# Optimization experiments

Hardware: AMD Instinct MI355X
Metric: run time of the kernel (lower is better)

The kernel has to match this reference:

```python
import jax, jax.numpy as jnp
import numpy as np


def setup_inputs() -> dict:
    key = jax.random.key(0)
    k1, k2, k3, k4 = jax.random.split(key, 4)
    B, S, D = 32, 2048, 128
    queries = jax.random.normal(k1, (B, S, D), dtype=jnp.float32)
    keys = jax.random.normal(k2, (B, S, D), dtype=jnp.float32)
    values = jax.random.normal(k3, (B, S, D), dtype=jnp.float32)
    mask = jax.random.randint(k4, (B, 1, S), 0, 2, dtype=jnp.int32)
    return {"queries": queries, "keys": keys, "values": values, "mask": mask}


def reference(queries, keys, values, mask):
    # scores: [B, Sq, Sk]
    scores = jnp.einsum("bqd,bkd->bqk", queries, keys)
    pad = (mask == 0)  # broadcasts [B,1,Sk] over queries
    min_value = jnp.finfo(scores.dtype).min
    scores = jnp.where(pad, min_value, scores)
    attn = jax.nn.softmax(scores, axis=-1)
    attn = jnp.where(pad, jnp.array(0.0, attn.dtype), attn)
    return jnp.einsum("bqk,bkd->bqd", attn, values)
```

## Files before the change

### kernel.cpp

```cpp
#include <hip/hip_runtime.h>
#include <stdint.h>

#define Bb 32
#define Ss 2048
#define Dd 128
#define KVB 64
#define NIT (Ss / KVB)

typedef __attribute__((ext_vector_type(2))) float f32x2;
typedef __attribute__((ext_vector_type(4))) float f32x4;
typedef __attribute__((ext_vector_type(16))) float f32x16;
typedef __attribute__((ext_vector_type(8))) _Float16 f16x8;
typedef __attribute__((ext_vector_type(2))) __fp16 fp16x2;
typedef __attribute__((ext_vector_type(8))) unsigned short u16x8;
typedef __attribute__((ext_vector_type(4))) unsigned short u16x4;

union F16_8 { u16x8 u; uint32_t w[4]; f16x8 h; };
union F16_4 { u16x4 u; uint32_t w[2]; };

__device__ __forceinline__ uint32_t pk2(float a, float b) {
    union { fp16x2 h; uint32_t u; } v;
    v.h = __builtin_amdgcn_cvt_pkrtz(a, b);
    return v.u;
}

__global__ __launch_bounds__(256)
void attn_prep(const float* __restrict__ K, const float* __restrict__ V,
               const int* __restrict__ M,
               unsigned short* __restrict__ Kc, unsigned short* __restrict__ Vc,
               int* __restrict__ CNT) {
    __shared__ int scan_s[256];
    __shared__ unsigned short idx_l[Ss];
    const int b = blockIdx.x >> 5, chunk = blockIdx.x & 31;
    const int tid = threadIdx.x;

    const int* m = M + (size_t)b * Ss + tid * 8;
    int loc[8]; int csum = 0;
    {
        int4 a = *(const int4*)m;
        int4 c = *(const int4*)(m + 4);
        loc[0] = (a.x != 0); loc[1] = (a.y != 0); loc[2] = (a.z != 0); loc[3] = (a.w != 0);
        loc[4] = (c.x != 0); loc[5] = (c.y != 0); loc[6] = (c.z != 0); loc[7] = (c.w != 0);
#pragma unroll
        for (int j = 0; j < 8; ++j) csum += loc[j];
    }
    scan_s[tid] = csum;
    __syncthreads();
    for (int off = 1; off < 256; off <<= 1) {
        int v = scan_s[tid];
        int u = (tid >= off) ? scan_s[tid - off] : 0;
        __syncthreads();
        scan_s[tid] = v + u;
        __syncthreads();
    }
    const int count = scan_s[255];
    {
        int base = scan_s[tid] - csum;
#pragma unroll
        for (int j = 0; j < 8; ++j)
            if (loc[j]) idx_l[base++] = (unsigned short)(tid * 8 + j);
    }
    __syncthreads();
    if (chunk == 0 && tid == 0) CNT[b] = count;

    const int ntpad = ((count + 63) >> 6) << 6;
    const int p0 = chunk * 64;
    if (p0 >= ntpad) return;

    const int rsub = tid >> 4;
    const int colh = (tid & 15) * 8;
    const size_t gbase = (size_t)b * Ss * Dd;
#pragma unroll
    for (int pass = 0; pass < 2; ++pass) {
        const float* src = pass ? V : K;
        unsigned short* dst = pass ? Vc : Kc;
#pragma unroll
        for (int it = 0; it < 4; ++it) {
            int s = p0 + rsub + it * 16;
            if (s >= ntpad) continue;
            F16_8 t;
            if (s < count) {
                const float* sp = src + gbase + (size_t)idx_l[s] * Dd + colh;
                f32x4 x = *(const f32x4*)sp;
                f32x4 y = *(const f32x4*)(sp + 4);
                t.w[0] = pk2(x[0], x[1]); t.w[1] = pk2(x[2], x[3]);
                t.w[2] = pk2(y[0], y[1]); t.w[3] = pk2(y[2], y[3]);
            } else {
                t.w[0] = 0u; t.w[1] = 0u; t.w[2] = 0u; t.w[3] = 0u;
            }
            *(u16x8*)(dst + gbase + (size_t)s * Dd + colh) = t.u;
        }
    }
}

__global__ __launch_bounds__(256) __attribute__((amdgpu_waves_per_eu(2, 2)))
void attn_fwd_d(const float* __restrict__ Q,
                const unsigned short* __restrict__ Kc,
                const unsigned short* __restrict__ Vc,
                const int* __restrict__ CNT,
                float* __restrict__ O) {
    __shared__ unsigned short K_lds[2][KVB * 128];
    __shared__ unsigned short VT_lds[2][128 * 64];
    __shared__ float maskadd[KVB];

    const int tid = threadIdx.x;
    const int w   = tid >> 6;
    const int l   = tid & 63;
    const int q31 = l & 31;
    const int hi  = l >> 5;

    const int bid   = blockIdx.x;
    const int batch = (bid & 7) * 4 + (bid >> 7);
    const int qtile = (bid >> 3) & 15;

    const size_t qrow0 = (size_t)batch * Ss + qtile * 128 + w * 32;
    const size_t kvb16 = (size_t)batch * Ss * Dd;

    const int count = CNT[batch];
    const int ntile = (count + KVB - 1) >> 6;

    const int grow = tid >> 4;
    const int gs   = tid & 15;
    auto gloadK = [&](int bf, int kv) {
#pragma unroll
        for (int it = 0; it < 4; ++it) {
            const int r = it * 16 + grow;
            const unsigned short* src = Kc + kvb16 + (size_t)(kv + r) * Dd + ((gs ^ (r & 7)) << 3);
            void* dst = (char*)(&K_lds[bf][0]) + it * 4096 + w * 1024;
            __builtin_amdgcn_global_load_lds(
                (const __attribute__((address_space(1))) uint32_t*)src,
                (__attribute__((address_space(3))) uint32_t*)dst, 16, 0, 0);
        }
    };

    const int vi = tid & 15;
    const int vk = (tid >> 4) << 2;
    uint32_t vv[4][4];

    auto issueV = [&](int kv) {
#pragma unroll
        for (int j = 0; j < 4; ++j)
#pragma unroll
            for (int ko = 0; ko < 4; ++ko)
                vv[j][ko] = *(const uint32_t*)(Vc + kvb16 + (size_t)(kv + vk + ko) * Dd + 2 * vi + 32 * j);
    };
    auto writeV = [&](int bf) {
#pragma unroll
        for (int j = 0; j < 4; ++j)
#pragma unroll
            for (int p = 0; p < 2; ++p) {
                int row = 2 * vi + p + 32 * j;
                F16_4 t;
                if (p == 0) {
                    t.w[0] = (vv[j][0] & 0xffffu) | (vv[j][1] << 16);
                    t.w[1] = (vv[j][2] & 0xffffu) | (vv[j][3] << 16);
                } else {
                    t.w[0] = (vv[j][0] >> 16) | (vv[j][1] & 0xffff0000u);
                    t.w[1] = (vv[j][2] >> 16) | (vv[j][3] & 0xffff0000u);
                }
                *(u16x4*)&VT_lds[bf][row * 64 + (vk ^ ((row & 7) << 3))] = t.u;
            }
    };

    F16_8 ones;
    {
        uint32_t ow = (q31 < 8) ? 0x3C003C00u : 0u;
        ones.w[0] = ow; ones.w[1] = ow; ones.w[2] = ow; ones.w[3] = ow;
    }

    const f32x16 z16 = {0,0,0,0,0,0,0,0,0,0,0,0,0,0,0,0};
    f32x16 acco[4];
#pragma unroll
    for (int dn = 0; dn < 4; ++dn) acco[dn] = z16;
    f32x16 accl = z16;
    float mrun = -1e4f;

    const float LOG2E = 1.44269504088896340736f;
    if (ntile > 0) { gloadK(0, 0); issueV(0); }
    if (tid < KVB) maskadd[tid] = ((ntile - 1) * KVB + tid < count) ? 0.f : -1e30f;
    F16_8 qf[8];
#pragma unroll
    for (int ks = 0; ks < 8; ++ks) {
        const float* s = Q + (qrow0 + q31) * Dd + ks * 16 + hi * 8;
        f32x4 a = *(const f32x4*)s;
        f32x4 b = *(const f32x4*)(s + 4);
        qf[ks].w[0] = pk2(a[0] * LOG2E, a[1] * LOG2E);
        qf[ks].w[1] = pk2(a[2] * LOG2E, a[3] * LOG2E);
        qf[ks].w[2] = pk2(b[0] * LOG2E, b[1] * LOG2E);
        qf[ks].w[3] = pk2(b[2] * LOG2E, b[3] * LOG2E);
    }
    if (ntile > 0) {
        writeV(0);
        __syncthreads();
    }

    for (int t = 0; t < ntile; ++t) {
        const int bf = t & 1;
        const bool pf = (t + 1 < ntile);
        if (pf) { gloadK(bf ^ 1, (t + 1) * KVB); issueV((t + 1) * KVB); }

        f32x16 accs[2];
        accs[0] = z16; accs[1] = z16;
#pragma unroll
        for (int ks = 0; ks < 8; ++ks) {
#pragma unroll
            for (int n = 0; n < 2; ++n) {
                int row = n * 32 + q31;
                F16_8 kf;
                kf.u = *(const u16x8*)&K_lds[bf][(row * 128 + ks * 16 + hi * 8) ^ ((row & 7) << 3)];
                accs[n] = __builtin_amdgcn_mfma_f32_32x32x16_f16(kf.h, qf[ks].h, accs[n], 0, 0, 0);
            }
        }

        if ((t == ntile - 1) && (count & 63)) {
#pragma unroll
            for (int n = 0; n < 2; ++n)
#pragma unroll
                for (int blk = 0; blk < 4; ++blk) {
                    f32x4 md = *(const f32x4*)&maskadd[n * 32 + blk * 8 + 4 * hi];
#pragma unroll
                    for (int r = 0; r < 4; ++r) accs[n][blk * 4 + r] += md[r];
                }
        }

        float mx[16];
#pragma unroll
        for (int i = 0; i < 16; ++i) mx[i] = fmaxf(accs[0][i], accs[1][i]);
#pragma unroll
        for (int s = 8; s >= 1; s >>= 1)
#pragma unroll
            for (int i = 0; i < s; ++i) mx[i] = fmaxf(mx[i], mx[i + s]);
        float pmax = fmaxf(mx[0], __shfl_xor(mx[0], 32));

        if (!__all(pmax - mrun <= 11.5409f)) {
            float mnew = fmaxf(mrun, pmax);
            float sc = __builtin_amdgcn_exp2f(mrun - mnew);
#pragma unroll
            for (int dn = 0; dn < 4; ++dn)
#pragma unroll
                for (int i = 0; i < 16; ++i) acco[dn][i] *= sc;
            accl[0] *= sc;
            mrun = mnew;
        }

#pragma unroll
        for (int n = 0; n < 2; ++n)
#pragma unroll
            for (int i = 0; i < 16; ++i) accs[n][i] = __builtin_amdgcn_exp2f(accs[n][i] - mrun);

        F16_8 pa[4];
#pragma unroll
        for (int ks = 0; ks < 4; ++ks) {
            int n  = ks >> 1;
            int b4 = (ks & 1) * 8;
            uint32_t x0 = pk2(accs[n][b4 + 0], accs[n][b4 + 1]);
            uint32_t x1 = pk2(accs[n][b4 + 2], accs[n][b4 + 3]);
            uint32_t y0 = pk2(accs[n][b4 + 4], accs[n][b4 + 5]);
            uint32_t y1 = pk2(accs[n][b4 + 6], accs[n][b4 + 7]);
            asm volatile("v_permlane32_swap_b32 %0, %1" : "+v"(x0), "+v"(y0));
            asm volatile("v_permlane32_swap_b32 %0, %1" : "+v"(x1), "+v"(y1));
            pa[ks].w[0] = x0; pa[ks].w[1] = x1; pa[ks].w[2] = y0; pa[ks].w[3] = y1;
        }

        if (pf) writeV(bf ^ 1);

#pragma unroll
        for (int dn = 0; dn < 4; ++dn) {
            int row = dn * 32 + q31;
#pragma unroll
            for (int ks = 0; ks < 4; ++ks) {
                F16_8 vf;
                vf.u = *(const u16x8*)&VT_lds[bf][row * 64 + ((ks * 16 + hi * 8) ^ ((row & 7) << 3))];
                acco[dn] = __builtin_amdgcn_mfma_f32_32x32x16_f16(vf.h, pa[ks].h, acco[dn], 0, 0, 0);
            }
        }
#pragma unroll
        for (int ks = 0; ks < 4; ++ks)
            accl = __builtin_amdgcn_mfma_f32_32x32x16_f16(ones.h, pa[ks].h, accl, 0, 0, 0);

        if (pf) __syncthreads();
    }

    float lv   = accl[0];
    float linv = lv > 0.f ? 1.0f / lv : 0.f;
    float* orow = O + (qrow0 + q31) * Dd;
#pragma unroll
    for (int dn = 0; dn < 4; ++dn)
#pragma unroll
        for (int rg = 0; rg < 4; ++rg) {
            f32x4 o;
            o[0] = acco[dn][rg * 4 + 0] * linv;
            o[1] = acco[dn][rg * 4 + 1] * linv;
            o[2] = acco[dn][rg * 4 + 2] * linv;
            o[3] = acco[dn][rg * 4 + 3] * linv;
            *(f32x4*)(orow + dn * 32 + rg * 8 + 4 * hi) = o;
        }
}

__global__ __launch_bounds__(256) __attribute__((amdgpu_waves_per_eu(2, 2)))
void attn_fwd(const float* __restrict__ Q,
              const float* __restrict__ K,
              const float* __restrict__ V,
              const int* __restrict__ M,
              float* __restrict__ O) {
    __shared__ unsigned short K_lds[KVB * 128];
    __shared__ unsigned short VT_lds[128 * 64];
    __shared__ float maskadd[KVB];

    const int tid = threadIdx.x;
    const int w   = tid >> 6;
    const int l   = tid & 63;
    const int q31 = l & 31;
    const int hi  = l >> 5;

    const int bid   = blockIdx.x;
    const int batch = (bid & 7) * 4 + (bid >> 7);
    const int qtile = (bid >> 3) & 15;

    const size_t qrow0  = (size_t)batch * Ss + qtile * 128 + w * 32;
    const size_t kvbase = (size_t)batch * Ss * Dd;
    const size_t mbase  = (size_t)batch * Ss;

    const int krow = tid >> 4;
    const int kcol = (tid & 15) << 3;
    const int vi   = tid & 15;
    const int vk   = (tid >> 4) << 2;

    f32x4 ka[4], kb[4];
    f32x2 vv[4][4];
    int mld = 0;

    auto issueK = [&](int kv) {
#pragma unroll
        for (int it = 0; it < 4; ++it) {
            const float* s = K + kvbase + (size_t)(kv + krow + it * 16) * Dd + kcol;
            ka[it] = *(const f32x4*)s;
            kb[it] = *(const f32x4*)(s + 4);
        }
        if (tid < KVB) mld = M[mbase + kv + tid];
    };
    auto writeK = [&]() {
#pragma unroll
        for (int it = 0; it < 4; ++it) {
            int row = krow + it * 16;
            F16_8 t;
            t.w[0] = pk2(ka[it][0], ka[it][1]);
            t.w[1] = pk2(ka[it][2], ka[it][3]);
            t.w[2] = pk2(kb[it][0], kb[it][1]);
            t.w[3] = pk2(kb[it][2], kb[it][3]);
            *(u16x8*)&K_lds[(row * 128 + kcol) ^ ((row & 7) << 3)] = t.u;
        }
        if (tid < KVB) maskadd[tid] = mld ? 0.f : -1e30f;
    };
    auto issueV = [&](int kv) {
#pragma unroll
        for (int j = 0; j < 4; ++j)
#pragma unroll
            for (int ko = 0; ko < 4; ++ko)
                vv[j][ko] = *(const f32x2*)(V + kvbase + (size_t)(kv + vk + ko) * Dd + 2 * vi + 32 * j);
    };
    auto writeV = [&]() {
#pragma unroll
        for (int j = 0; j < 4; ++j)
#pragma unroll
            for (int p = 0; p < 2; ++p) {
                int row = 2 * vi + p + 32 * j;
                F16_4 t;
                t.w[0] = pk2(vv[j][0][p], vv[j][1][p]);
                t.w[1] = pk2(vv[j][2][p], vv[j][3][p]);
                *(u16x4*)&VT_lds[row * 64 + (vk ^ ((row & 7) << 3))] = t.u;
            }
    };

    F16_8 ones;
    {
        uint32_t ow = (q31 < 8) ? 0x3C003C00u : 0u;
        ones.w[0] = ow; ones.w[1] = ow; ones.w[2] = ow; ones.w[3] = ow;
    }

    const f32x16 z16 = {0,0,0,0,0,0,0,0,0,0,0,0,0,0,0,0};
    f32x16 acco[4];
#pragma unroll
    for (int dn = 0; dn < 4; ++dn) acco[dn] = z16;
    f32x16 accl = z16;
    float mrun = -1e4f;

    const float LOG2E = 1.44269504088896340736f;
    issueK(0); issueV(0);
    F16_8 qf[8];
#pragma unroll
    for (int ks = 0; ks < 8; ++ks) {
        const float* s = Q + (qrow0 + q31) * Dd + ks * 16 + hi * 8;
        f32x4 a = *(const f32x4*)s;
        f32x4 b = *(const f32x4*)(s + 4);
        qf[ks].w[0] = pk2(a[0] * LOG2E, a[1] * LOG2E);
        qf[ks].w[1] = pk2(a[2] * LOG2E, a[3] * LOG2E);
        qf[ks].w[2] = pk2(b[0] * LOG2E, b[1] * LOG2E);
        qf[ks].w[3] = pk2(b[2] * LOG2E, b[3] * LOG2E);
    }
    writeK(); writeV();
    __syncthreads();

    for (int t = 0; t < NIT; ++t) {
        if (t < NIT - 1) issueK((t + 1) * KVB);

        f32x16 accs[2];
        accs[0] = z16; accs[1] = z16;
#pragma unroll
        for (int ks = 0; ks < 8; ++ks) {
#pragma unroll
            for (int n = 0; n < 2; ++n) {
                int row = n * 32 + q31;
                F16_8 kf;
                kf.u = *(const u16x8*)&K_lds[(row * 128 + ks * 16 + hi * 8) ^ ((row & 7) << 3)];
                accs[n] = __builtin_amdgcn_mfma_f32_32x32x16_f16(kf.h, qf[ks].h, accs[n], 0, 0, 0);
            }
        }

#pragma unroll
        for (int n = 0; n < 2; ++n)
#pragma unroll
            for (int blk = 0; blk < 4; ++blk) {
                f32x4 md = *(const f32x4*)&maskadd[n * 32 + blk * 8 + 4 * hi];
#pragma unroll
                for (int r = 0; r < 4; ++r) accs[n][blk * 4 + r] += md[r];
            }

        float mx[16];
#pragma unroll
        for (int i = 0; i < 16; ++i) mx[i] = fmaxf(accs[0][i], accs[1][i]);
#pragma unroll
        for (int s = 8; s >= 1; s >>= 1)
#pragma unroll
            for (int i = 0; i < s; ++i) mx[i] = fmaxf(mx[i], mx[i + s]);
        float pmax = fmaxf(mx[0], __shfl_xor(mx[0], 32));

        if (!__all(pmax - mrun <= 11.5409f)) {
            float mnew = fmaxf(mrun, pmax);
            float sc = __builtin_amdgcn_exp2f(mrun - mnew);
#pragma unroll
            for (int dn = 0; dn < 4; ++dn)
#pragma unroll
                for (int i = 0; i < 16; ++i) acco[dn][i] *= sc;
            accl[0] *= sc;
            mrun = mnew;
        }

#pragma unroll
        for (int n = 0; n < 2; ++n)
#pragma unroll
            for (int i = 0; i < 16; ++i) accs[n][i] = __builtin_amdgcn_exp2f(accs[n][i] - mrun);

        F16_8 pa[4];
#pragma unroll
        for (int ks = 0; ks < 4; ++ks) {
            int n  = ks >> 1;
            int b4 = (ks & 1) * 8;
            uint32_t x0 = pk2(accs[n][b4 + 0], accs[n][b4 + 1]);
            uint32_t x1 = pk2(accs[n][b4 + 2], accs[n][b4 + 3]);
            uint32_t y0 = pk2(accs[n][b4 + 4], accs[n][b4 + 5]);
            uint32_t y1 = pk2(accs[n][b4 + 6], accs[n][b4 + 7]);
            asm volatile("v_permlane32_swap_b32 %0, %1" : "+v"(x0), "+v"(y0));
            asm volatile("v_permlane32_swap_b32 %0, %1" : "+v"(x1), "+v"(y1));
            pa[ks].w[0] = x0; pa[ks].w[1] = x1; pa[ks].w[2] = y0; pa[ks].w[3] = y1;
        }

        __syncthreads();
        if (t < NIT - 1) { writeK(); issueV((t + 1) * KVB); }

#pragma unroll
        for (int dn = 0; dn < 4; ++dn) {
            int row = dn * 32 + q31;
#pragma unroll
            for (int ks = 0; ks < 4; ++ks) {
                F16_8 vf;
                vf.u = *(const u16x8*)&VT_lds[row * 64 + ((ks * 16 + hi * 8) ^ ((row & 7) << 3))];
                acco[dn] = __builtin_amdgcn_mfma_f32_32x32x16_f16(vf.h, pa[ks].h, acco[dn], 0, 0, 0);
            }
        }
#pragma unroll
        for (int ks = 0; ks < 4; ++ks)
            accl = __builtin_amdgcn_mfma_f32_32x32x16_f16(ones.h, pa[ks].h, accl, 0, 0, 0);

        __syncthreads();
        if (t < NIT - 1) writeV();
    }

    float lv   = accl[0];
    float linv = lv > 0.f ? 1.0f / lv : 0.f;
    float* orow = O + (qrow0 + q31) * Dd;
#pragma unroll
    for (int dn = 0; dn < 4; ++dn)
#pragma unroll
        for (int rg = 0; rg < 4; ++rg) {
            f32x4 o;
            o[0] = acco[dn][rg * 4 + 0] * linv;
            o[1] = acco[dn][rg * 4 + 1] * linv;
            o[2] = acco[dn][rg * 4 + 2] * linv;
            o[3] = acco[dn][rg * 4 + 3] * linv;
            *(f32x4*)(orow + dn * 32 + rg * 8 + 4 * hi) = o;
        }
}

extern "C" void kernel_launch(void* const* d_in, const int* in_sizes, int n_in,
                              void* d_out, int out_size, void* d_ws, size_t ws_size,
                              hipStream_t stream) {
    const float* Q = (const float*)d_in[0];
    const float* K = (const float*)d_in[1];
    const float* V = (const float*)d_in[2];
    const int*   M = (const int*)d_in[3];
    float* O = (float*)d_out;

    const size_t nKV  = (size_t)Bb * Ss * Dd;
    const size_t need = nKV * 2 * 2 + (size_t)Bb * 4;

    if (d_ws != nullptr && ws_size >= need) {
        unsigned short* Kc  = (unsigned short*)d_ws;
        unsigned short* Vc  = Kc + nKV;
        int*            CNT = (int*)(Vc + nKV);
        attn_prep<<<dim3(Bb * 32), dim3(256), 0, stream>>>(K, V, M, Kc, Vc, CNT);
        attn_fwd_d<<<dim3(Bb * (Ss / 128)), dim3(256), 0, stream>>>(Q, Kc, Vc, CNT, O);
    } else {
        attn_fwd<<<dim3(Bb * (Ss / 128)), dim3(256), 0, stream>>>(Q, K, V, M, O);
    }
}
```

Before: 69.61 us.

## Pre-pack K and V into MFMA fragment order in prep kernel

The prep kernel now writes compacted K and V tiles directly in the per-lane MFMA fragment layout, with V transposed through shared memory. The attention kernel then loads both tiles with direct global-to-LDS copies and reads fragments at linear offsets. This removes the register staging and in-kernel V transpose, the swizzle arithmetic, and the mask-add LDS array, which is replaced by a per-element compare. The cost is a heavier prep kernel with an LDS transpose that has strided 16-bit reads likely to hit bank conflicts, plus a remapped batch order in prep.

```diff
diff --git a/kernel.cpp b/kernel.cpp
--- a/kernel.cpp
+++ b/kernel.cpp
@@ -27,11 +27,15 @@
 __global__ __launch_bounds__(256)
 void attn_prep(const float* __restrict__ K, const float* __restrict__ V,
                const int* __restrict__ M,
-               unsigned short* __restrict__ Kc, unsigned short* __restrict__ Vc,
+               unsigned short* __restrict__ Kf, unsigned short* __restrict__ Vf,
                int* __restrict__ CNT) {
     __shared__ int scan_s[256];
     __shared__ unsigned short idx_l[Ss];
-    const int b = blockIdx.x >> 5, chunk = blockIdx.x & 31;
+    __shared__ unsigned short vt[KVB * 128];
+
+    const int x = blockIdx.x;
+    const int b     = ((x & 7) << 2) | ((x >> 3) & 3);
+    const int chunk = x >> 5;
     const int tid = threadIdx.x;
 
     const int* m = M + (size_t)b * Ss + tid * 8;
@@ -63,45 +67,79 @@
     __syncthreads();
     if (chunk == 0 && tid == 0) CNT[b] = count;
 
-    const int ntpad = ((count + 63) >> 6) << 6;
-    const int p0 = chunk * 64;
-    if (p0 >= ntpad) return;
-
-    const int rsub = tid >> 4;
-    const int colh = (tid & 15) * 8;
+    const int ntile = (count + 63) >> 6;
+    if (chunk >= ntile) return;
+
+    const int kb = chunk * 64;
     const size_t gbase = (size_t)b * Ss * Dd;
-#pragma unroll
-    for (int pass = 0; pass < 2; ++pass) {
-        const float* src = pass ? V : K;
-        unsigned short* dst = pass ? Vc : Kc;
+    const size_t fbase = ((size_t)b * 32 + chunk) * 8192;
+
+#pragma unroll
+    for (int j = 0; j < 4; ++j) {
+        const int o  = tid + 256 * j;
+        const int l  = o & 63;
+        const int fn = o >> 6;
+        const int ks = fn >> 1, n = fn & 1;
+        const int s  = kb + n * 32 + (l & 31);
+        const int d0 = ks * 16 + (l >> 5) * 8;
+        F16_8 t;
+        if (s < count) {
+            const float* sp = K + gbase + (size_t)idx_l[s] * Dd + d0;
+            f32x4 xv = *(const f32x4*)sp;
+            f32x4 yv = *(const f32x4*)(sp + 4);
+            t.w[0] = pk2(xv[0], xv[1]); t.w[1] = pk2(xv[2], xv[3]);
+            t.w[2] = pk2(yv[0], yv[1]); t.w[3] = pk2(yv[2], yv[3]);
+        } else {
+            t.w[0] = 0u; t.w[1] = 0u; t.w[2] = 0u; t.w[3] = 0u;
+        }
+        *(u16x8*)(Kf + fbase + (size_t)o * 8) = t.u;
+    }
+
+    {
+        const int rsub = tid >> 4;
+        const int colh = (tid & 15) * 8;
 #pragma unroll
         for (int it = 0; it < 4; ++it) {
-            int s = p0 + rsub + it * 16;
-            if (s >= ntpad) continue;
+            const int row = rsub + it * 16;
+            const int s   = kb + row;
             F16_8 t;
             if (s < count) {
-                const float* sp = src + gbase + (size_t)idx_l[s] * Dd + colh;
-                f32x4 x = *(const f32x4*)sp;
-                f32x4 y = *(const f32x4*)(sp + 4);
-                t.w[0] = pk2(x[0], x[1]); t.w[1] = pk2(x[2], x[3]);
-                t.w[2] = pk2(y[0], y[1]); t.w[3] = pk2(y[2], y[3]);
+                const float* sp = V + gbase + (size_t)idx_l[s] * Dd + colh;
+                f32x4 xv = *(const f32x4*)sp;
+                f32x4 yv = *(const f32x4*)(sp + 4);
+                t.w[0] = pk2(xv[0], xv[1]); t.w[1] = pk2(xv[2], xv[3]);
+                t.w[2] = pk2(yv[0], yv[1]); t.w[3] = pk2(yv[2], yv[3]);
             } else {
                 t.w[0] = 0u; t.w[1] = 0u; t.w[2] = 0u; t.w[3] = 0u;
             }
-            *(u16x8*)(dst + gbase + (size_t)s * Dd + colh) = t.u;
-        }
+            *(u16x8*)&vt[row * 128 + colh] = t.u;
+        }
+    }
+    __syncthreads();
+
+#pragma unroll
+    for (int j = 0; j < 4; ++j) {
+        const int o  = tid + 256 * j;
+        const int l  = o & 63;
+        const int fn = o >> 6;
+        const int dn = fn >> 2, ks = fn & 3;
+        const int d  = dn * 32 + (l & 31);
+        const int k0 = ks * 16 + (l >> 5) * 8;
+        u16x8 t;
+#pragma unroll
+        for (int jj = 0; jj < 8; ++jj) t[jj] = vt[(k0 + jj) * 128 + d];
+        *(u16x8*)(Vf + fbase + (size_t)o * 8) = t;
     }
 }
 
 __global__ __launch_bounds__(256) __attribute__((amdgpu_waves_per_eu(2, 2)))
-void attn_fwd_d(const float* __restrict__ Q,
-                const unsigned short* __restrict__ Kc,
-                const unsigned short* __restrict__ Vc,
+void attn_fwd_f(const float* __restrict__ Q,
+                const unsigned short* __restrict__ Kf,
+                const unsigned short* __restrict__ Vf,
                 const int* __restrict__ CNT,
                 float* __restrict__ O) {
-    __shared__ unsigned short K_lds[2][KVB * 128];
-    __shared__ unsigned short VT_lds[2][128 * 64];
-    __shared__ float maskadd[KVB];
+    __shared__ unsigned short K_lds[2][8192];
+    __shared__ unsigned short V_lds[2][8192];
 
     const int tid = threadIdx.x;
     const int w   = tid >> 6;
@@ -114,52 +152,21 @@
     const int qtile = (bid >> 3) & 15;
 
     const size_t qrow0 = (size_t)batch * Ss + qtile * 128 + w * 32;
-    const size_t kvb16 = (size_t)batch * Ss * Dd;
+    const size_t kfb   = (size_t)batch * 32 * 8192;
 
     const int count = CNT[batch];
     const int ntile = (count + KVB - 1) >> 6;
 
-    const int grow = tid >> 4;
-    const int gs   = tid & 15;
-    auto gloadK = [&](int bf, int kv) {
+    auto gload = [&](int kv_t, const unsigned short* base, unsigned short (&dstb)[8192]) {
 #pragma unroll
         for (int it = 0; it < 4; ++it) {
-            const int r = it * 16 + grow;
-            const unsigned short* src = Kc + kvb16 + (size_t)(kv + r) * Dd + ((gs ^ (r & 7)) << 3);
-            void* dst = (char*)(&K_lds[bf][0]) + it * 4096 + w * 1024;
+            const int ob = it * 4096 + w * 1024;
+            const unsigned short* src = base + (size_t)kv_t * 8192 + (ob >> 1) + l * 8;
+            void* dst = (char*)&dstb[0] + ob;
             __builtin_amdgcn_global_load_lds(
                 (const __attribute__((address_space(1))) uint32_t*)src,
                 (__attribute__((address_space(3))) uint32_t*)dst, 16, 0, 0);
         }
-    };
-
-    const int vi = tid & 15;
-    const int vk = (tid >> 4) << 2;
-    uint32_t vv[4][4];
-
-    auto issueV = [&](int kv) {
-#pragma unroll
-        for (int j = 0; j < 4; ++j)
-#pragma unroll
-            for (int ko = 0; ko < 4; ++ko)
-                vv[j][ko] = *(const uint32_t*)(Vc + kvb16 + (size_t)(kv + vk + ko) * Dd + 2 * vi + 32 * j);
-    };
-    auto writeV = [&](int bf) {
-#pragma unroll
-        for (int j = 0; j < 4; ++j)
-#pragma unroll
-            for (int p = 0; p < 2; ++p) {
-                int row = 2 * vi + p + 32 * j;
-                F16_4 t;
-                if (p == 0) {
-                    t.w[0] = (vv[j][0] & 0xffffu) | (vv[j][1] << 16);
-                    t.w[1] = (vv[j][2] & 0xffffu) | (vv[j][3] << 16);
-                } else {
-                    t.w[0] = (vv[j][0] >> 16) | (vv[j][1] & 0xffff0000u);
-                    t.w[1] = (vv[j][2] >> 16) | (vv[j][3] & 0xffff0000u);
-                }
-                *(u16x4*)&VT_lds[bf][row * 64 + (vk ^ ((row & 7) << 3))] = t.u;
-            }
     };
 
     F16_8 ones;
@@ -176,8 +183,7 @@
     float mrun = -1e4f;
 
     const float LOG2E = 1.44269504088896340736f;
-    if (ntile > 0) { gloadK(0, 0); issueV(0); }
-    if (tid < KVB) maskadd[tid] = ((ntile - 1) * KVB + tid < count) ? 0.f : -1e30f;
+    if (ntile > 0) { gload(0, Kf + kfb, K_lds[0]); gload(0, Vf + kfb, V_lds[0]); }
     F16_8 qf[8];
 #pragma unroll
     for (int ks = 0; ks < 8; ++ks) {
@@ -189,37 +195,39 @@
         qf[ks].w[2] = pk2(b[0] * LOG2E, b[1] * LOG2E);
         qf[ks].w[3] = pk2(b[2] * LOG2E, b[3] * LOG2E);
     }
-    if (ntile > 0) {
-        writeV(0);
-        __syncthreads();
-    }
+    if (ntile > 0) __syncthreads();
+
+    const int lb = l * 16;
 
     for (int t = 0; t < ntile; ++t) {
         const int bf = t & 1;
         const bool pf = (t + 1 < ntile);
-        if (pf) { gloadK(bf ^ 1, (t + 1) * KVB); issueV((t + 1) * KVB); }
+        if (pf) {
+            gload(t + 1, Kf + kfb, K_lds[bf ^ 1]);
+            gload(t + 1, Vf + kfb, V_lds[bf ^ 1]);
+        }
 
         f32x16 accs[2];
         accs[0] = z16; accs[1] = z16;
+        const char* kl = (const char*)&K_lds[bf][0];
 #pragma unroll
         for (int ks = 0; ks < 8; ++ks) {
 #pragma unroll
             for (int n = 0; n < 2; ++n) {
-                int row = n * 32 + q31;
                 F16_8 kf;
-                kf.u = *(const u16x8*)&K_lds[bf][(row * 128 + ks * 16 + hi * 8) ^ ((row & 7) << 3)];
+                kf.u = *(const u16x8*)(kl + (ks * 2 + n) * 1024 + lb);
                 accs[n] = __builtin_amdgcn_mfma_f32_32x32x16_f16(kf.h, qf[ks].h, accs[n], 0, 0, 0);
             }
         }
 
         if ((t == ntile - 1) && (count & 63)) {
+            const int rem = count - t * 64;
 #pragma unroll
             for (int n = 0; n < 2; ++n)
 #pragma unroll
-                for (int blk = 0; blk < 4; ++blk) {
-                    f32x4 md = *(const f32x4*)&maskadd[n * 32 + blk * 8 + 4 * hi];
-#pragma unroll
-                    for (int r = 0; r < 4; ++r) accs[n][blk * 4 + r] += md[r];
+                for (int i = 0; i < 16; ++i) {
+                    const int key = n * 32 + (i >> 2) * 8 + 4 * hi + (i & 3);
+                    accs[n][i] = (key < rem) ? accs[n][i] : -1e30f;
                 }
         }
 
@@ -262,15 +270,13 @@
             pa[ks].w[0] = x0; pa[ks].w[1] = x1; pa[ks].w[2] = y0; pa[ks].w[3] = y1;
         }
 
-        if (pf) writeV(bf ^ 1);
-
+        const char* vl = (const char*)&V_lds[bf][0];
 #pragma unroll
         for (int dn = 0; dn < 4; ++dn) {
-            int row = dn * 32 + q31;
 #pragma unroll
             for (int ks = 0; ks < 4; ++ks) {
                 F16_8 vf;
-                vf.u = *(const u16x8*)&VT_lds[bf][row * 64 + ((ks * 16 + hi * 8) ^ ((row & 7) << 3))];
+                vf.u = *(const u16x8*)(vl + (dn * 4 + ks) * 1024 + lb);
                 acco[dn] = __builtin_amdgcn_mfma_f32_32x32x16_f16(vf.h, pa[ks].h, acco[dn], 0, 0, 0);
             }
         }
@@ -511,15 +517,15 @@
     const int*   M = (const int*)d_in[3];
     float* O = (float*)d_out;
 
-    const size_t nKV  = (size_t)Bb * Ss * Dd;
-    const size_t need = nKV * 2 * 2 + (size_t)Bb * 4;
+    const size_t nF   = (size_t)Bb * 32 * 8192;
+    const size_t need = nF * 2 * 2 + (size_t)Bb * 4;
 
     if (d_ws != nullptr && ws_size >= need) {
-        unsigned short* Kc  = (unsigned short*)d_ws;
-        unsigned short* Vc  = Kc + nKV;
-        int*            CNT = (int*)(Vc + nKV);
-        attn_prep<<<dim3(Bb * 32), dim3(256), 0, stream>>>(K, V, M, Kc, Vc, CNT);
-        attn_fwd_d<<<dim3(Bb * (Ss / 128)), dim3(256), 0, stream>>>(Q, Kc, Vc, CNT, O);
+        unsigned short* Kf  = (unsigned short*)d_ws;
+        unsigned short* Vf  = Kf + nF;
+        int*            CNT = (int*)(Vf + nF);
+        attn_prep<<<dim3(Bb * 32), dim3(256), 0, stream>>>(K, V, M, Kf, Vf, CNT);
+        attn_fwd_f<<<dim3(Bb * (Ss / 128)), dim3(256), 0, stream>>>(Q, Kf, Vf, CNT, O);
     } else {
         attn_fwd<<<dim3(Bb * (Ss / 128)), dim3(256), 0, stream>>>(Q, K, V, M, O);
     }
```

Measured after the change: 65.72 us. 1.06x faster.
